# Performance work log

Measured on AMD Instinct MI355X. Metric: run time of the kernel, lower is better.

## Reference

```python
import jax, jax.numpy as jnp
import numpy as np

B, S = 2, 2048          # 2 prompt sequences of 2048 tokens (packed: T = B*S)
H, KV, D, G = 32, 8, 128, 128   # heads, kv heads, head_dim, quant group size
THETA = 1e6


def _dequant(w_int, scales, g=G):
    # w_int: [O, I] int4 values in [-8, 7]; scales: [O, I//g] per-group fp scales
    return w_int.astype(jnp.float32) * jnp.repeat(scales, g, axis=1)


def _rope_neox(x, pos):
    # x: [B, S, h, D]; pos: [B, S]; neox style rotates (first half, second half)
    half = D // 2
    inv_freq = 1.0 / (THETA ** (jnp.arange(half, dtype=jnp.float32) / half))
    ang = pos[:, :, None] * inv_freq[None, None, :]          # [B, S, half]
    cos = jnp.cos(ang)[:, :, None, :]
    sin = jnp.sin(ang)[:, :, None, :]
    x1, x2 = x[..., :half], x[..., half:]
    return jnp.concatenate([x1 * cos - x2 * sin, x2 * cos + x1 * sin], axis=-1)


def setup_inputs() -> dict:
    key = jax.random.key(0)
    k1, k2, k3, k4, k5, k6 = jax.random.split(key, 6)
    T, HID = B * S, H * D
    q_hidden = jax.random.randint(k1, (T, HID), -127, 128, dtype=jnp.int32)  # int8 acts
    q_scale = jax.random.uniform(k2, (T,), dtype=jnp.float32) * 0.01 + 1e-4  # per-token scale
    q_sum = jnp.sum(q_hidden, axis=-1).astype(jnp.float32)                   # per-token int8 sum
    OUT_QKV = (H + 2 * KV) * D
    w_qkv = jax.random.randint(k3, (OUT_QKV, HID), -8, 8, dtype=jnp.int32)   # int4 weights
    s_qkv = jax.random.uniform(k4, (OUT_QKV, HID // G), dtype=jnp.float32) * 0.01 + 1e-4
    w_o = jax.random.randint(k5, (HID, HID), -8, 8, dtype=jnp.int32)
    s_o = jax.random.uniform(k6, (HID, HID // G), dtype=jnp.float32) * 0.01 + 1e-4
    return {"q_hidden": q_hidden, "q_scale": q_scale, "q_sum": q_sum,
            "w_qkv": w_qkv, "s_qkv": s_qkv, "w_o": w_o, "s_o": s_o}


def reference(q_hidden, q_scale, q_sum, w_qkv, s_qkv, w_o, s_o):
    T = q_hidden.shape[0]
    # W4A8 qkv_proj with dynamic per-token input scale (symmetric int4 -> sum unused)
    x = q_hidden.astype(jnp.float32) * q_scale[:, None]          # dequant activations
    qkv = x @ _dequant(w_qkv, s_qkv).T                            # [T, (H+2KV)*D]
    q_sz, kv_sz = H * D, KV * D
    q = qkv[:, :q_sz].reshape(B, S, H, D)
    k = qkv[:, q_sz:q_sz + kv_sz].reshape(B, S, KV, D)
    v = qkv[:, q_sz + kv_sz:].reshape(B, S, KV, D)
    # fused bias(none)+RoPE (neox, full head_dim)
    pos = jnp.broadcast_to(jnp.arange(S, dtype=jnp.float32), (B, S))
    q = _rope_neox(q, pos)
    k = _rope_neox(k, pos)
    # varlen causal flash attention (GQA: 4 q-heads per kv head)
    qg = q.reshape(B, S, KV, H // KV, D)
    scores = jnp.einsum('bsghd,btgd->bghst', qg, k) * (D ** -0.5)
    causal = jnp.tril(jnp.ones((S, S), dtype=bool))
    scores = jnp.where(causal[None, None, None], scores, -jnp.inf)
    p = jax.nn.softmax(scores, axis=-1)
    attn = jnp.einsum('bghst,btgd->bsghd', p, v).reshape(T, H * D)
    # invoke_quant_fuse_sum: per-token symmetric int8 requant of attn output
    amax = jnp.maximum(jnp.max(jnp.abs(attn), axis=-1, keepdims=True), 1e-6)
    a_scale = amax / 127.0
    attn_q = jnp.clip(jnp.round(attn / a_scale), -127.0, 127.0)
    # W4A8 o_proj
    out = (attn_q * a_scale) @ _dequant(w_o, s_o).T               # [T, H*D]
    return out
```

## Files before the change

kernel.cpp:

```cpp
#include <hip/hip_runtime.h>
#include <math.h>

#define B_ 2
#define S_ 2048
#define H_ 32
#define KV_ 8
#define D_ 128
#define T_ 4096
#define HID_ 4096
#define OQKV_ 6144

typedef __attribute__((ext_vector_type(4))) float f32x4;
typedef __attribute__((ext_vector_type(4))) int i32x4;
typedef __attribute__((ext_vector_type(8))) __bf16 bf16x8;
typedef __attribute__((ext_vector_type(8))) unsigned short u16x8;
typedef unsigned short u16;
typedef signed char s8;

__device__ __forceinline__ u16 f2b(float f) {
  unsigned x = __float_as_uint(f);
  return (u16)((x + 0x7FFFu + ((x >> 16) & 1u)) >> 16);
}
__device__ __forceinline__ float b2f(u16 u) {
  return __uint_as_float(((unsigned)u) << 16);
}

__device__ __forceinline__ void async16(const void* g, void* l) {
  __builtin_amdgcn_global_load_lds((__attribute__((address_space(1))) void*)g,
                                   (__attribute__((address_space(3))) void*)l,
                                   16, 0, 0);
}

__device__ __forceinline__ bf16x8 ld8(const u16* p) { return *(const bf16x8*)p; }

__device__ __forceinline__ f32x4 mfma16x16(bf16x8 a, bf16x8 b, f32x4 c) {
  return __builtin_amdgcn_mfma_f32_16x16x32_bf16(a, b, c, 0, 0, 0);
}

__device__ __forceinline__ bf16x8 ones8() {
  union { u16x8 u; bf16x8 b; } c;
  c.u = u16x8{0x3F80, 0x3F80, 0x3F80, 0x3F80, 0x3F80, 0x3F80, 0x3F80, 0x3F80};
  return c.b;
}

__global__ __launch_bounds__(256) void pack_i8(const int* __restrict__ w,
                                               s8* __restrict__ out) {
  size_t base = ((size_t)blockIdx.x * 256 + threadIdx.x) * 4;
  int4 v = *(const int4*)(w + base);
  unsigned r = (unsigned)(v.x & 255) | ((unsigned)(v.y & 255) << 8) |
               ((unsigned)(v.z & 255) << 16) | ((unsigned)v.w << 24);
  *(unsigned*)(out + base) = r;
}

__global__ __launch_bounds__(256) void rope_kernel(u16* __restrict__ qkv) {
  int idx = blockIdx.x * 256 + threadIdx.x;
  int t = idx / 2560;
  int r = idx - t * 2560;
  int head = r >> 6;
  int d = r & 63;
  int col = (head < 32) ? (head * 128 + d) : (4096 + (head - 32) * 128 + d);
  size_t base = (size_t)t * 6144 + col;
  float x1 = b2f(qkv[base]);
  float x2 = b2f(qkv[base + 64]);
  float e = (float)d * 0.015625f;
  float freq = exp2f(e * -19.931568569324174f);
  float ang = (float)(t & 2047) * freq;
  float sn, cs;
  sincosf(ang, &sn, &cs);
  qkv[base] = f2b(x1 * cs - x2 * sn);
  qkv[base + 64] = f2b(x2 * cs + x1 * sn);
}

__global__ __launch_bounds__(256) void vt_transpose(const u16* __restrict__ qkv,
                                                    u16* __restrict__ vt) {
  __shared__ u16 tile[64][65];
  const int s0 = blockIdx.x * 64, d0 = blockIdx.y * 64;
  const int bk = blockIdx.z, b = bk >> 3, kv = bk & 7;
  const int tid = threadIdx.x;
  const int rr = tid >> 3, cc = tid & 7;
#pragma unroll
  for (int it = 0; it < 2; it++) {
    int r = it * 32 + rr;
    u16x8 v = *(const u16x8*)(qkv + (size_t)(b * 2048 + s0 + r) * 6144 + 5120 +
                              kv * 128 + d0 + cc * 8);
#pragma unroll
    for (int k = 0; k < 8; k++) tile[r][cc * 8 + k] = v[k];
  }
  __syncthreads();
#pragma unroll
  for (int it = 0; it < 2; it++) {
    int d = it * 32 + rr;
    u16x8 o;
#pragma unroll
    for (int k = 0; k < 8; k++) o[k] = tile[cc * 8 + k][d];
    *(u16x8*)(vt + (size_t)(bk * 128 + d0 + d) * 2048 + s0 + cc * 8) = o;
  }
}

__device__ __forceinline__ void store_out(float* p, float v) { *p = v; }
__device__ __forceinline__ void store_out(u16* p, float v) { *p = f2b(v); }

template <typename OutT>
__global__ __launch_bounds__(256) void gemm_i8(const s8* __restrict__ A,
                                               const s8* __restrict__ Bw,
                                               const float* __restrict__ sB,
                                               const float* __restrict__ rowscale,
                                               OutT* __restrict__ C,
                                               int M, int N, int K) {
  __shared__ __align__(16) s8 As[128 * 64];
  __shared__ __align__(16) s8 Bs[128 * 64];
  __shared__ float Ss[128][33];
  const int tid = threadIdx.x;
  const int lane = tid & 63;
  const int wv = tid >> 6;
  const int wm = wv >> 1, wn = wv & 1;
  const int m0 = blockIdx.y * 128, n0 = blockIdx.x * 128;
  const int g = lane >> 4, c15 = lane & 15;
  const int KG = K >> 7;

  for (int i = tid; i < 128 * 32; i += 256)
    Ss[i >> 5][i & 31] = sB[(size_t)n0 * 32 + i];

  f32x4 acc[4][4] = {};

  const int c0 = 2 * wv, c1 = c0 + 1;
  const int srow = lane >> 2;
  const int pch = lane & 3;
  const int scol = (((pch - (srow >> 1)) & 3)) * 16;
  const s8* Ag0 = A + (size_t)(m0 + c0 * 16 + srow) * K + scol;
  const s8* Ag1 = A + (size_t)(m0 + c1 * 16 + srow) * K + scol;
  const s8* Bg0 = Bw + (size_t)(n0 + c0 * 16 + srow) * K + scol;
  const s8* Bg1 = Bw + (size_t)(n0 + c1 * 16 + srow) * K + scol;
  s8* Al0 = As + c0 * 1024 + lane * 16;
  s8* Al1 = As + c1 * 1024 + lane * 16;
  s8* Bl0 = Bs + c0 * 1024 + lane * 16;
  s8* Bl1 = Bs + c1 * 1024 + lane * 16;

  for (int grp = 0; grp < KG; grp++) {
    i32x4 iacc[4][4];
#pragma unroll
    for (int sub = 0; sub < 2; sub++) {
      const int kb = grp * 128 + sub * 64;
      __syncthreads();
      async16(Ag0 + kb, Al0);
      async16(Ag1 + kb, Al1);
      async16(Bg0 + kb, Bl0);
      async16(Bg1 + kb, Bl1);
      __syncthreads();
      i32x4 af[4], bf[4];
#pragma unroll
      for (int i = 0; i < 4; i++) {
        af[i] = *(const i32x4*)(As + (wm * 64 + i * 16 + c15) * 64 +
                                ((g + (c15 >> 1)) & 3) * 16);
        bf[i] = *(const i32x4*)(Bs + (wn * 64 + i * 16 + c15) * 64 +
                                ((g + (c15 >> 1)) & 3) * 16);
      }
#pragma unroll
      for (int i = 0; i < 4; i++)
#pragma unroll
        for (int j = 0; j < 4; j++)
          iacc[i][j] = __builtin_amdgcn_mfma_i32_16x16x64_i8(
              af[i], bf[j], sub ? iacc[i][j] : (i32x4){0, 0, 0, 0}, 0, 0, 0);
    }
#pragma unroll
    for (int j = 0; j < 4; j++) {
      const float sc = Ss[wn * 64 + j * 16 + c15][grp];
#pragma unroll
      for (int i = 0; i < 4; i++)
#pragma unroll
        for (int r = 0; r < 4; r++)
          acc[i][j][r] += sc * (float)iacc[i][j][r];
    }
  }

#pragma unroll
  for (int i = 0; i < 4; i++) {
#pragma unroll
    for (int r = 0; r < 4; r++) {
      int m = m0 + wm * 64 + i * 16 + g * 4 + r;
      float scm = rowscale[m];
#pragma unroll
      for (int j = 0; j < 4; j++) {
        int n = n0 + wn * 64 + j * 16 + c15;
        store_out(C + (size_t)m * N + n, acc[i][j][r] * scm);
      }
    }
  }
}


struct AttnState {
  f32x4 acc[2][9];
  float mrun[2][4];
};

template <bool FULL>
__device__ __forceinline__ void qk_phase(int j0, int q0w, const u16* Ksp,
                                         const bf16x8 qf[2][4],
                                         f32x4 (&sc)[2][4], int g, int c15) {
  const int qmax = q0w + 31;
#pragma unroll
  for (int nt = 0; nt < 4; nt++) {
    if (FULL || (j0 + nt * 16 <= qmax)) {
      bf16x8 kf[4];
#pragma unroll
      for (int c = 0; c < 4; c++)
        kf[c] = ld8(Ksp + (nt * 16 + c15) * 128 +
                    (((g + 4 * c) ^ (c15 & 7)) * 8));
      f32x4 s0 = {0.f, 0.f, 0.f, 0.f}, s1 = {0.f, 0.f, 0.f, 0.f};
#pragma unroll
      for (int c = 0; c < 4; c++) {
        s0 = mfma16x16(qf[0][c], kf[c], s0);
        s1 = mfma16x16(qf[1][c], kf[c], s1);
      }
      if (FULL) {
#pragma unroll
        for (int r = 0; r < 4; r++) {
          sc[0][nt][r] = s0[r] * 0.08838834764831845f;
          sc[1][nt][r] = s1[r] * 0.08838834764831845f;
        }
      } else {
        const int key = j0 + nt * 16 + c15;
#pragma unroll
        for (int r = 0; r < 4; r++) {
          sc[0][nt][r] =
              (key <= q0w + g * 4 + r) ? s0[r] * 0.08838834764831845f : -INFINITY;
          sc[1][nt][r] =
              (key <= q0w + 16 + g * 4 + r) ? s1[r] * 0.08838834764831845f : -INFINITY;
        }
      }
    }
  }
}

template <bool FULL>
__device__ __forceinline__ void smax_pv(int j0, int q0w, const u16* Vsp,
                                        u16* pw0, u16* pw1, f32x4 (&sc)[2][4],
                                        AttnState& st, int g, int c15,
                                        const bf16x8 vones) {
  const int qmax = q0w + 31;
#pragma unroll
  for (int m = 0; m < 2; m++) {
    u16* pw = m ? pw1 : pw0;
    float alpha[4];
#pragma unroll
    for (int r = 0; r < 4; r++) {
      float rm = -INFINITY;
#pragma unroll
      for (int nt = 0; nt < 4; nt++)
        if (FULL || (j0 + nt * 16 <= qmax)) rm = fmaxf(rm, sc[m][nt][r]);
      rm = fmaxf(rm, __shfl_xor(rm, 1));
      rm = fmaxf(rm, __shfl_xor(rm, 2));
      rm = fmaxf(rm, __shfl_xor(rm, 4));
      rm = fmaxf(rm, __shfl_xor(rm, 8));
      float mnew = fmaxf(st.mrun[m][r], rm);
      alpha[r] = __expf(st.mrun[m][r] - mnew);
      st.mrun[m][r] = mnew;
#pragma unroll
      for (int nt = 0; nt < 4; nt++) {
        float pv = (FULL || (j0 + nt * 16 <= qmax))
                       ? __expf(sc[m][nt][r] - mnew) : 0.0f;
        pw[(g * 4 + r) * 72 + nt * 16 + c15] = f2b(pv);
      }
    }
#pragma unroll
    for (int dt = 0; dt < 9; dt++)
#pragma unroll
      for (int r = 0; r < 4; r++) st.acc[m][dt][r] *= alpha[r];
  }
#pragma unroll
  for (int kc = 0; kc < 2; kc++) {
    bf16x8 pf0 = ld8(pw0 + c15 * 72 + kc * 32 + g * 8);
    bf16x8 pf1 = ld8(pw1 + c15 * 72 + kc * 32 + g * 8);
#pragma unroll
    for (int dt = 0; dt < 8; dt++) {
      bf16x8 vf = ld8(Vsp + (dt * 16 + c15) * 64 +
                      (((g + 4 * kc) ^ (c15 & 7)) * 8));
      st.acc[0][dt] = mfma16x16(pf0, vf, st.acc[0][dt]);
      st.acc[1][dt] = mfma16x16(pf1, vf, st.acc[1][dt]);
    }
    st.acc[0][8] = mfma16x16(pf0, vones, st.acc[0][8]);
    st.acc[1][8] = mfma16x16(pf1, vones, st.acc[1][8]);
  }
}

__global__ __launch_bounds__(256, 2) void attn_kernel(const u16* __restrict__ qkvb,
                                                      const u16* __restrict__ vtb,
                                                      float* __restrict__ out) {
  __shared__ __align__(16) u16 Ks[64 * 128];
  __shared__ __align__(16) u16 Vs[2][128 * 64];
  __shared__ __align__(16) u16 Ps[4][2][16 * 72];
  const int tid = threadIdx.x, lane = tid & 63, wv = tid >> 6;
  const int g = lane >> 4, c15 = lane & 15;
  const int h = blockIdx.x, b = blockIdx.y, qb = 15 - (int)blockIdx.z;
  const int kvh = h >> 2;
  const int Q0 = qb * 128;
  const int q0w = Q0 + wv * 32;
  const int nsteps = 2 * qb + 2;
  const bf16x8 vones = ones8();
  u16* pw0 = &Ps[wv][0][0];
  u16* pw1 = &Ps[wv][1][0];

  const int keyl = lane >> 4, kch = lane & 15;
  const int dll = lane >> 3, vch = lane & 7;
  const u16* Kg = qkvb + (size_t)(b * 2048) * 6144 + 4096 + kvh * 128;
  const u16* Vg = vtb + (size_t)((b * 8 + kvh) * 128) * 2048;

  auto stageK = [&](int j0) {
#pragma unroll
    for (int i = 0; i < 4; i++) {
      const int key = wv * 16 + i * 4 + keyl;
      async16(Kg + (size_t)(j0 + key) * 6144 + ((kch ^ (key & 7)) * 8),
              (u16*)Ks + (wv * 16 + i * 4) * 128 + lane * 8);
    }
  };
  auto stageV = [&](int j0, int vb) {
#pragma unroll
    for (int i = 0; i < 4; i++) {
      const int d = wv * 32 + i * 8 + dll;
      async16(Vg + (size_t)d * 2048 + j0 + ((vch ^ (d & 7)) * 8),
              (u16*)&Vs[vb][0] + (wv * 32 + i * 8) * 64 + lane * 8);
    }
  };

  bf16x8 qf[2][4];
#pragma unroll
  for (int m = 0; m < 2; m++) {
    const u16* qp =
        qkvb + (size_t)(b * 2048 + q0w + m * 16 + c15) * 6144 + h * 128 + g * 8;
#pragma unroll
    for (int c = 0; c < 4; c++) qf[m][c] = ld8(qp + c * 32);
  }

  AttnState st;
#pragma unroll
  for (int m = 0; m < 2; m++) {
#pragma unroll
    for (int dt = 0; dt < 9; dt++) st.acc[m][dt] = f32x4{0.f, 0.f, 0.f, 0.f};
#pragma unroll
    for (int r = 0; r < 4; r++) st.mrun[m][r] = -INFINITY;
  }

  stageK(0);
  stageV(0, 0);

  for (int jt = 0; jt < nsteps; ++jt) {
    const int j0 = jt * 64;
    __syncthreads();
    const int mode = (j0 + 64 <= q0w) ? 0 : ((j0 <= q0w + 31) ? 1 : 2);
    f32x4 sc[2][4];
    if (mode == 0) qk_phase<true>(j0, q0w, (const u16*)Ks, qf, sc, g, c15);
    else if (mode == 1) qk_phase<false>(j0, q0w, (const u16*)Ks, qf, sc, g, c15);
    __syncthreads();
    if (jt + 1 < nsteps) {
      stageK(j0 + 64);
      stageV(j0 + 64, (jt + 1) & 1);
    }
    const u16* Vsp = (const u16*)&Vs[jt & 1][0];
    if (mode == 0) smax_pv<true>(j0, q0w, Vsp, pw0, pw1, sc, st, g, c15, vones);
    else if (mode == 1) smax_pv<false>(j0, q0w, Vsp, pw0, pw1, sc, st, g, c15, vones);
  }

#pragma unroll
  for (int m = 0; m < 2; m++)
#pragma unroll
    for (int r = 0; r < 4; r++) {
      const int row = q0w + m * 16 + g * 4 + r;
      float inv = 1.0f / st.acc[m][8][r];
      float* op = out + (size_t)(b * 2048 + row) * 4096 + h * 128;
#pragma unroll
      for (int dt = 0; dt < 8; dt++) op[dt * 16 + c15] = st.acc[m][dt][r] * inv;
    }
}

__global__ __launch_bounds__(256) void quant_kernel(const float* __restrict__ attn,
                                                    s8* __restrict__ aq,
                                                    float* __restrict__ ascale) {
  const int t = blockIdx.x, tid = threadIdx.x;
  const float* row = attn + (size_t)t * 4096;
  f32x4 v[4];
  float am = 0.f;
#pragma unroll
  for (int i = 0; i < 4; i++) {
    v[i] = *(const f32x4*)(row + tid * 16 + i * 4);
#pragma unroll
    for (int r = 0; r < 4; r++) am = fmaxf(am, fabsf(v[i][r]));
  }
#pragma unroll
  for (int m = 1; m <= 32; m <<= 1) am = fmaxf(am, __shfl_xor(am, m));
  __shared__ float red[4];
  if ((tid & 63) == 0) red[tid >> 6] = am;
  __syncthreads();
  am = fmaxf(fmaxf(red[0], red[1]), fmaxf(red[2], red[3]));
  float asc = fmaxf(am, 1e-6f) / 127.0f;
  if (tid == 0) ascale[t] = asc;
  int w[4];
#pragma unroll
  for (int i = 0; i < 4; i++) {
    int bytes[4];
#pragma unroll
    for (int r = 0; r < 4; r++) {
      float q = rintf(v[i][r] / asc);
      q = fminf(127.0f, fmaxf(-127.0f, q));
      bytes[r] = ((int)q) & 255;
    }
    w[i] = bytes[0] | (bytes[1] << 8) | (bytes[2] << 16) | (bytes[3] << 24);
  }
  *(int4*)(aq + (size_t)t * 4096 + tid * 16) = int4{w[0], w[1], w[2], w[3]};
}

extern "C" void kernel_launch(void* const* d_in, const int* in_sizes, int n_in,
                              void* d_out, int out_size, void* d_ws, size_t ws_size,
                              hipStream_t stream) {
  const int* q_hidden = (const int*)d_in[0];
  const float* q_scale = (const float*)d_in[1];
  const int* w_qkv = (const int*)d_in[3];
  const float* s_qkv = (const float*)d_in[4];
  const int* w_o = (const int*)d_in[5];
  const float* s_o = (const float*)d_in[6];
  float* out = (float*)d_out;

  char* ws = (char*)d_ws;
  const size_t MB = 1024 * 1024;
  s8* WB = (s8*)(ws);
  u16* QKVB = (u16*)(ws + 48 * MB);
  u16* VTB = (u16*)(ws);
  s8* ATTNQ = (s8*)(ws + 8 * MB);
  float* ASC = (float*)(ws + 25 * MB);
  s8* WOB = (s8*)(ws + 48 * MB);
  s8* XB = (s8*)d_out;

  pack_i8<<<16384, 256, 0, stream>>>(q_hidden, XB);
  pack_i8<<<24576, 256, 0, stream>>>(w_qkv, WB);
  gemm_i8<u16><<<dim3(48, 32), 256, 0, stream>>>(XB, WB, s_qkv, q_scale, QKVB,
                                                 T_, OQKV_, HID_);
  rope_kernel<<<40960, 256, 0, stream>>>(QKVB);
  vt_transpose<<<dim3(32, 2, 16), 256, 0, stream>>>(QKVB, VTB);
  attn_kernel<<<dim3(32, 2, 16), 256, 0, stream>>>(QKVB, VTB, out);
  quant_kernel<<<4096, 256, 0, stream>>>(out, ATTNQ, ASC);
  pack_i8<<<16384, 256, 0, stream>>>(w_o, WOB);
  gemm_i8<float><<<dim3(32, 32), 256, 0, stream>>>(ATTNQ, WOB, s_o, ASC, out,
                                                   T_, HID_, HID_);
}
```

Measured before the change: 693.9 us.

## Double-buffer LDS tiles in int8 GEMM to overlap loads with MFMA

```diff
diff --git a/kernel.cpp b/kernel.cpp
--- a/kernel.cpp
+++ b/kernel.cpp
@@ -107,8 +107,8 @@
                                                const float* __restrict__ rowscale,
                                                OutT* __restrict__ C,
                                                int M, int N, int K) {
-  __shared__ __align__(16) s8 As[128 * 64];
-  __shared__ __align__(16) s8 Bs[128 * 64];
+  __shared__ __align__(16) s8 As[2][128 * 64];
+  __shared__ __align__(16) s8 Bs[2][128 * 64];
   __shared__ float Ss[128][33];
   const int tid = threadIdx.x;
   const int lane = tid & 63;
@@ -116,7 +116,7 @@
   const int wm = wv >> 1, wn = wv & 1;
   const int m0 = blockIdx.y * 128, n0 = blockIdx.x * 128;
   const int g = lane >> 4, c15 = lane & 15;
-  const int KG = K >> 7;
+  const int NS = K >> 6;
 
   for (int i = tid; i < 128 * 32; i += 256)
     Ss[i >> 5][i & 31] = sB[(size_t)n0 * 32 + i];
@@ -131,46 +131,51 @@
   const s8* Ag1 = A + (size_t)(m0 + c1 * 16 + srow) * K + scol;
   const s8* Bg0 = Bw + (size_t)(n0 + c0 * 16 + srow) * K + scol;
   const s8* Bg1 = Bw + (size_t)(n0 + c1 * 16 + srow) * K + scol;
-  s8* Al0 = As + c0 * 1024 + lane * 16;
-  s8* Al1 = As + c1 * 1024 + lane * 16;
-  s8* Bl0 = Bs + c0 * 1024 + lane * 16;
-  s8* Bl1 = Bs + c1 * 1024 + lane * 16;
-
-  for (int grp = 0; grp < KG; grp++) {
-    i32x4 iacc[4][4];
-#pragma unroll
-    for (int sub = 0; sub < 2; sub++) {
-      const int kb = grp * 128 + sub * 64;
-      __syncthreads();
-      async16(Ag0 + kb, Al0);
-      async16(Ag1 + kb, Al1);
-      async16(Bg0 + kb, Bl0);
-      async16(Bg1 + kb, Bl1);
-      __syncthreads();
-      i32x4 af[4], bf[4];
-#pragma unroll
-      for (int i = 0; i < 4; i++) {
-        af[i] = *(const i32x4*)(As + (wm * 64 + i * 16 + c15) * 64 +
-                                ((g + (c15 >> 1)) & 3) * 16);
-        bf[i] = *(const i32x4*)(Bs + (wn * 64 + i * 16 + c15) * 64 +
-                                ((g + (c15 >> 1)) & 3) * 16);
+  const int l0 = c0 * 1024 + lane * 16;
+  const int l1 = c1 * 1024 + lane * 16;
+
+  auto stage = [&](int kb, int buf) {
+    async16(Ag0 + kb, &As[buf][0] + l0);
+    async16(Ag1 + kb, &As[buf][0] + l1);
+    async16(Bg0 + kb, &Bs[buf][0] + l0);
+    async16(Bg1 + kb, &Bs[buf][0] + l1);
+  };
+
+  stage(0, 0);
+  __syncthreads();
+
+  i32x4 iacc[4][4];
+  for (int step = 0; step < NS; ++step) {
+    const int cur = step & 1;
+    if (step + 1 < NS) stage((step + 1) << 6, cur ^ 1);
+    i32x4 af[4], bf[4];
+#pragma unroll
+    for (int i = 0; i < 4; i++) {
+      af[i] = *(const i32x4*)(&As[cur][0] + (wm * 64 + i * 16 + c15) * 64 +
+                              ((g + (c15 >> 1)) & 3) * 16);
+      bf[i] = *(const i32x4*)(&Bs[cur][0] + (wn * 64 + i * 16 + c15) * 64 +
+                              ((g + (c15 >> 1)) & 3) * 16);
+    }
+    const int sub = step & 1;
+#pragma unroll
+    for (int i = 0; i < 4; i++)
+#pragma unroll
+      for (int j = 0; j < 4; j++)
+        iacc[i][j] = __builtin_amdgcn_mfma_i32_16x16x64_i8(
+            af[i], bf[j], sub ? iacc[i][j] : (i32x4){0, 0, 0, 0}, 0, 0, 0);
+    if (sub) {
+      const int grp = step >> 1;
+#pragma unroll
+      for (int j = 0; j < 4; j++) {
+        const float sc = Ss[wn * 64 + j * 16 + c15][grp];
+#pragma unroll
+        for (int i = 0; i < 4; i++)
+#pragma unroll
+          for (int r = 0; r < 4; r++)
+            acc[i][j][r] += sc * (float)iacc[i][j][r];
       }
-#pragma unroll
-      for (int i = 0; i < 4; i++)
-#pragma unroll
-        for (int j = 0; j < 4; j++)
-          iacc[i][j] = __builtin_amdgcn_mfma_i32_16x16x64_i8(
-              af[i], bf[j], sub ? iacc[i][j] : (i32x4){0, 0, 0, 0}, 0, 0, 0);
-    }
-#pragma unroll
-    for (int j = 0; j < 4; j++) {
-      const float sc = Ss[wn * 64 + j * 16 + c15][grp];
-#pragma unroll
-      for (int i = 0; i < 4; i++)
-#pragma unroll
-        for (int r = 0; r < 4; r++)
-          acc[i][j][r] += sc * (float)iacc[i][j][r];
-    }
+    }
+    __syncthreads();
   }
 
 #pragma unroll
```

Result: slower. 841.3 us (+21.2%).
